# Performance work log

Measured on AMD Instinct MI355X. Metric: run time of the kernel, lower is better.

The kernel has to match this reference:

```python
import jax, jax.numpy as jnp
import numpy as np

B_, L_, H_ = 8, 512, 768
DIN, N, R, K = 1536, 64, 48, 4  # d_inner, d_state, dt_rank, d_conv


def setup_inputs() -> dict:
    key = jax.random.key(0)
    ks = jax.random.split(key, 16)
    rn = lambda i, shp, sc=0.02: jax.random.normal(ks[i], shp, dtype=jnp.float32) * sc
    inp = {
        "text": jax.random.normal(ks[0], (B_, L_, H_), dtype=jnp.float32),
        "audio": jax.random.normal(ks[1], (B_, L_, H_), dtype=jnp.float32),
        "video": jax.random.normal(ks[2], (B_, L_, H_), dtype=jnp.float32),
        "proj_w": rn(3, (3 * H_, H_)),
        "proj_b": jnp.zeros((H_,), jnp.float32),
        "proj_ln_g": jnp.ones((H_,), jnp.float32),
        "proj_ln_b": jnp.zeros((H_,), jnp.float32),
        "blk_ln_g": jnp.ones((H_,), jnp.float32),
        "blk_ln_b": jnp.zeros((H_,), jnp.float32),
        "in_proj_w": rn(4, (H_, 2 * DIN)),
        "conv_w": rn(5, (DIN, 1, K), 0.1),
        "conv_b": jnp.zeros((DIN,), jnp.float32),
        "x_proj_w": rn(6, (DIN, R + 2 * N)),
        "dt_proj_w": rn(7, (R, DIN), 0.1),
        "dt_proj_b": jnp.full((DIN,), -4.6, jnp.float32),  # softplus -> ~0.01 dt
        "A_log": jnp.log(jnp.tile(jnp.arange(1, N + 1, dtype=jnp.float32), (DIN, 1))),
        "D": jnp.ones((DIN,), jnp.float32),
        "out_proj_w": rn(8, (DIN, H_)),
    }
    return inp


def _ln(x, g, b, eps=1e-5):
    mu = x.mean(-1, keepdims=True)
    xc = x - mu
    v = (xc * xc).mean(-1, keepdims=True)
    return xc * jax.lax.rsqrt(v + eps) * g + b


def _mamba(h, in_proj_w, conv_w, conv_b, x_proj_w, dt_proj_w, dt_proj_b, A_log, D, out_proj_w):
    Bsz, L, _ = h.shape
    xz = h @ in_proj_w                       # [B,L,2*DIN]
    x, z = jnp.split(xz, 2, axis=-1)         # each [B,L,DIN]
    # causal depthwise conv1d over time
    xc = jax.lax.conv_general_dilated(
        x.transpose(0, 2, 1), conv_w, (1,), [(K - 1, 0)],
        dimension_numbers=("NCH", "OIH", "NCH"), feature_group_count=DIN)
    x = jax.nn.silu(xc + conv_b[None, :, None]).transpose(0, 2, 1)  # [B,L,DIN]
    dbl = x @ x_proj_w                       # [B,L,R+2N]
    dt, Bm, Cm = jnp.split(dbl, [R, R + N], axis=-1)
    delta = jax.nn.softplus(dt @ dt_proj_w + dt_proj_b)  # [B,L,DIN]
    A = -jnp.exp(A_log)                      # [DIN,N]

    def step(hcar, t):
        d_t, b_t, c_t, u_t = t               # [B,DIN],[B,N],[B,N],[B,DIN]
        hcar = jnp.exp(d_t[..., None] * A) * hcar + (d_t * u_t)[..., None] * b_t[:, None, :]
        y = jnp.einsum("bdn,bn->bd", hcar, c_t)
        return hcar, y

    xs = (delta.transpose(1, 0, 2), Bm.transpose(1, 0, 2), Cm.transpose(1, 0, 2), x.transpose(1, 0, 2))
    h0 = jnp.zeros((Bsz, DIN, N), x.dtype)
    _, ys = jax.lax.scan(step, h0, xs)       # ys: [L,B,DIN]
    y = ys.transpose(1, 0, 2) + x * D
    y = y * jax.nn.silu(z)
    return y @ out_proj_w                    # [B,L,H]


def reference(text, audio, video, proj_w, proj_b, proj_ln_g, proj_ln_b,
              blk_ln_g, blk_ln_b, in_proj_w, conv_w, conv_b, x_proj_w,
              dt_proj_w, dt_proj_b, A_log, D, out_proj_w):
    fused = jnp.concatenate([text, audio, video], axis=-1) @ proj_w + proj_b
    fused = _ln(fused, proj_ln_g, proj_ln_b)
    m = _mamba(_ln(fused, blk_ln_g, blk_ln_b), in_proj_w, conv_w, conv_b,
               x_proj_w, dt_proj_w, dt_proj_b, A_log, D, out_proj_w)
    fused = fused + m                         # residual (dropout = identity in eval)
    return fused.mean(axis=1)                 # [B,H]
```

## Files before the change

kernel.cpp:

```cpp
#include <hip/hip_runtime.h>
#include <hip/hip_bf16.h>
#include <cstddef>
#include <cstdint>

#define DIN 1536
#define LSEQ 512

typedef __hip_bfloat16 bf16;
typedef __attribute__((ext_vector_type(8))) short short8x;
typedef __attribute__((ext_vector_type(4))) float f32x4;
typedef const __attribute__((address_space(1))) unsigned int* gp1;
typedef __attribute__((address_space(3))) unsigned int* lp3;

__device__ inline float readlane_f(float v, int l) {
  return __uint_as_float(__builtin_amdgcn_readlane(__float_as_uint(v), l));
}
__device__ inline void gload_lds(const bf16* g, unsigned short* l) {
  __builtin_amdgcn_global_load_lds((gp1)g, (lp3)l, 16, 0, 0);
}
__device__ inline void bsplit(float v, bf16& h, bf16& l) {
  h = __float2bfloat16(v);
  l = __float2bfloat16(v - __bfloat162float(h));
}
__device__ inline float softplusf(float t) {
  return fmaxf(t, 0.f) + log1pf(__expf(-fabsf(t)));
}
template<int CTRL>
__device__ inline float dpp_add(float v) {
  int t = __builtin_amdgcn_update_dpp(0, __float_as_int(v), CTRL, 0xf, 0xf, true);
  return v + __int_as_float(t);
}
__device__ inline float dpp_wave_sum(float p) {
  p = dpp_add<0x111>(p);
  p = dpp_add<0x112>(p);
  p = dpp_add<0x114>(p);
  p = dpp_add<0x118>(p);
  p = dpp_add<0x142>(p);
  p = dpp_add<0x143>(p);
  return p;
}

template<int TBM, int TBN, int WR, int WC, int AMODE, int EPI>
__global__ __launch_bounds__(WR*WC*64) void mgemm(
    const bf16* __restrict__ Ah0, const bf16* __restrict__ Al0,
    const bf16* __restrict__ Ah1, const bf16* __restrict__ Al1,
    const bf16* __restrict__ Ah2, const bf16* __restrict__ Al2,
    const bf16* __restrict__ Bh, const bf16* __restrict__ Bl,
    const float* __restrict__ bias,
    float* __restrict__ C, float* __restrict__ C2,
    bf16* __restrict__ Oh, bf16* __restrict__ Ol,
    int K, int lda, int ldc)
{
  constexpr int NW = WR * WC;
  constexpr int SM = TBM / WR, SN = TBN / WC;
  constexpr int T_M = SM / 16, T_N = SN / 16;
  __shared__ unsigned short sAh[TBM * 32], sAl[TBM * 32];
  __shared__ unsigned short sBh[TBN * 32], sBl[TBN * 32];
  const int tid = threadIdx.x;
  const int lane = tid & 63, wid = tid >> 6;
  const int bm = blockIdx.x * TBM, bn = blockIdx.y * TBN;
  const int wr = wid / WC, wc = wid % WC;

  const int stg_m = lane >> 2;
  const int stg_k = ((lane & 3) ^ ((lane >> 3) & 3)) * 8;
  const int fo = (lane & 15) * 64 + ((((lane >> 4) ^ ((lane >> 1) & 3)) & 3) * 16);

  f32x4 acc[T_M][T_N];
  #pragma unroll
  for (int i = 0; i < T_M; ++i)
    #pragma unroll
    for (int j = 0; j < T_N; ++j) acc[i][j] = (f32x4){0.f, 0.f, 0.f, 0.f};

  for (int k0 = 0; k0 < K; k0 += 32) {
    __syncthreads();
    const bf16* pAh; const bf16* pAl; int ka;
    if (AMODE == 1) {
      int seg = k0 / 768;
      pAh = (seg == 0) ? Ah0 : (seg == 1) ? Ah1 : Ah2;
      pAl = (seg == 0) ? Al0 : (seg == 1) ? Al1 : Al2;
      ka = k0 - seg * 768;
    } else { pAh = Ah0; pAl = Al0; ka = k0; }
    #pragma unroll
    for (int q = wid; q < TBM / 16; q += NW) {
      size_t go = (size_t)(bm + q * 16 + stg_m) * lda + ka + stg_k;
      gload_lds(pAh + go, &sAh[q * 512]);
      gload_lds(pAl + go, &sAl[q * 512]);
    }
    #pragma unroll
    for (int q = wid; q < TBN / 16; q += NW) {
      size_t go = (size_t)(bn + q * 16 + stg_m) * K + k0 + stg_k;
      gload_lds(Bh + go, &sBh[q * 512]);
      gload_lds(Bl + go, &sBl[q * 512]);
    }
    __syncthreads();

    short8x ah[T_M], al[T_M], bh[T_N], bl[T_N];
    #pragma unroll
    for (int mi = 0; mi < T_M; ++mi) {
      int off = (wr * SM + mi * 16) * 64 + fo;
      ah[mi] = *(const short8x*)((const char*)sAh + off);
      al[mi] = *(const short8x*)((const char*)sAl + off);
    }
    #pragma unroll
    for (int nj = 0; nj < T_N; ++nj) {
      int off = (wc * SN + nj * 16) * 64 + fo;
      bh[nj] = *(const short8x*)((const char*)sBh + off);
      bl[nj] = *(const short8x*)((const char*)sBl + off);
    }
    #pragma unroll
    for (int mi = 0; mi < T_M; ++mi)
      #pragma unroll
      for (int nj = 0; nj < T_N; ++nj) {
        acc[mi][nj] = __builtin_amdgcn_mfma_f32_16x16x32_bf16(ah[mi], bh[nj], acc[mi][nj], 0, 0, 0);
        acc[mi][nj] = __builtin_amdgcn_mfma_f32_16x16x32_bf16(ah[mi], bl[nj], acc[mi][nj], 0, 0, 0);
        acc[mi][nj] = __builtin_amdgcn_mfma_f32_16x16x32_bf16(al[mi], bh[nj], acc[mi][nj], 0, 0, 0);
      }
  }

  const int cl = lane & 15, qd = lane >> 4;
  const int colbase = bn + wc * SN;
  const int rowbase = bm + wr * SM;
  if (EPI == 1) {
    #pragma unroll
    for (int mi = 0; mi < T_M; ++mi) {
      int r0 = rowbase + mi * 16 + qd * 4;
      #pragma unroll
      for (int nj = 0; nj < T_N; ++nj) {
        int col = colbase + nj * 16 + cl;
        float bv = bias[col];
        #pragma unroll
        for (int rg = 0; rg < 4; ++rg)
          C[(size_t)(r0 + rg) * ldc + col] = acc[mi][nj][rg] + bv;
      }
    }
  } else if (EPI == 4) {
    #pragma unroll
    for (int mi = 0; mi < T_M; ++mi) {
      int m = rowbase + mi * 16 + qd * 4;
      int b = m >> 9, l = m & 511;
      #pragma unroll
      for (int nj = 0; nj < T_N; ++nj) {
        int col = colbase + nj * 16 + cl;
        float bv = bias[col];
        float4 v;
        v.x = softplusf(acc[mi][nj][0] + bv);
        v.y = softplusf(acc[mi][nj][1] + bv);
        v.z = softplusf(acc[mi][nj][2] + bv);
        v.w = softplusf(acc[mi][nj][3] + bv);
        *reinterpret_cast<float4*>(&C[((size_t)b * DIN + col) * LSEQ + l]) = v;
      }
    }
  } else if (EPI == 5) {
    if (bn < 1536) {
      #pragma unroll
      for (int mi = 0; mi < T_M; ++mi) {
        int r0 = rowbase + mi * 16 + qd * 4;
        #pragma unroll
        for (int nj = 0; nj < T_N; ++nj) {
          int col = colbase + nj * 16 + cl;
          #pragma unroll
          for (int rg = 0; rg < 4; ++rg)
            C[(size_t)(r0 + rg) * ldc + col] = acc[mi][nj][rg];
        }
      }
    } else {
      #pragma unroll
      for (int mi = 0; mi < T_M; ++mi) {
        int m = rowbase + mi * 16 + qd * 4;
        int b = m >> 9, l = m & 511;
        #pragma unroll
        for (int nj = 0; nj < T_N; ++nj) {
          int colz = colbase - 1536 + nj * 16 + cl;
          float4 v;
          v.x = acc[mi][nj][0]; v.y = acc[mi][nj][1];
          v.z = acc[mi][nj][2]; v.w = acc[mi][nj][3];
          *reinterpret_cast<float4*>(&C2[((size_t)b * DIN + colz) * LSEQ + l]) = v;
        }
      }
    }
  } else if (EPI == 6) {
    #pragma unroll
    for (int mi = 0; mi < T_M; ++mi) {
      int r0 = rowbase + mi * 16 + qd * 4;
      #pragma unroll
      for (int nj = 0; nj < T_N; ++nj) {
        int col = colbase + nj * 16 + cl;
        #pragma unroll
        for (int rg = 0; rg < 4; ++rg) {
          float v = acc[mi][nj][rg];
          C[(size_t)(r0 + rg) * 192 + col] = v;
          if (col < 64) {
            bf16 h, l;
            if (col < 48) bsplit(v, h, l);
            else { h = __float2bfloat16(0.f); l = h; }
            Oh[(size_t)(r0 + rg) * 64 + col] = h;
            Ol[(size_t)(r0 + rg) * 64 + col] = l;
          }
        }
      }
    }
  }
}

__global__ __launch_bounds__(256) void split3_k(
    const float* __restrict__ s0, const float* __restrict__ s1,
    const float* __restrict__ s2, bf16* __restrict__ dst)
{
  const int per = 4096 * 768 / 256;
  int seg = blockIdx.x / per;
  int idx = (blockIdx.x - seg * per) * 256 + threadIdx.x;
  const float* src = (seg == 0) ? s0 : (seg == 1) ? s1 : s2;
  bf16* hi = dst + (size_t)seg * 2 * 4096 * 768;
  bf16* lo = hi + (size_t)4096 * 768;
  bf16 h, l; bsplit(src[idx], h, l);
  hi[idx] = h; lo[idx] = l;
}

__global__ __launch_bounds__(256) void wprep_k(
    const float* __restrict__ pw, const float* __restrict__ ipw,
    const float* __restrict__ xpw, const float* __restrict__ dtw,
    bf16* pwTh, bf16* pwTl, bf16* ipTh, bf16* ipTl,
    bf16* xpTh, bf16* xpTl, bf16* dtTh, bf16* dtTl)
{
  __shared__ float T[64][65];
  const int id = blockIdx.x, tid = threadIdx.x;
  const float* src; bf16 *hi, *lo; int P, Q, ld, Ppad, px, qx;
  if (id < 432)       { src = pw;  hi = pwTh; lo = pwTl; P = 2304; Q = 768;  ld = 768;  Ppad = 2304; px = id % 36;          qx = id / 36; }
  else if (id < 1008) { int i = id - 432;  src = ipw; hi = ipTh; lo = ipTl; P = 768;  Q = 3072; ld = 3072; Ppad = 768;  px = i % 12; qx = i / 12; }
  else if (id < 1080) { int i = id - 1008; src = xpw; hi = xpTh; lo = xpTl; P = 1536; Q = 176;  ld = 176;  Ppad = 1536; px = i % 24; qx = i / 24; }
  else                { int i = id - 1080; src = dtw; hi = dtTh; lo = dtTl; P = 48;   Q = 1536; ld = 1536; Ppad = 64;   px = 0;      qx = i; }
  const int p0 = px * 64, q0 = qx * 64;
  {
    int j = tid & 63, i0 = tid >> 6;
    for (int i = i0; i < 64; i += 4) {
      int p = p0 + i, q = q0 + j;
      T[i][j] = (p < P && q < Q) ? src[(size_t)p * ld + q] : 0.f;
    }
  }
  __syncthreads();
  {
    int ii = tid & 63, j0 = tid >> 6;
    for (int jj = j0; jj < 64; jj += 4) {
      bf16 h, l; bsplit(T[ii][jj], h, l);
      size_t o = (size_t)(q0 + jj) * Ppad + p0 + ii;
      hi[o] = h; lo[o] = l;
    }
  }
}

__device__ inline float block_sum256(float s, float* red) {
  #pragma unroll
  for (int o = 32; o > 0; o >>= 1) s += __shfl_xor(s, o, 64);
  int tid = threadIdx.x;
  __syncthreads();
  if ((tid & 63) == 0) red[tid >> 6] = s;
  __syncthreads();
  return red[0] + red[1] + red[2] + red[3];
}

__global__ __launch_bounds__(256) void ln2_k(
    const float* __restrict__ pre,
    const float* __restrict__ g1, const float* __restrict__ b1,
    const float* __restrict__ g2, const float* __restrict__ b2,
    float* __restrict__ fused, bf16* __restrict__ hAh, bf16* __restrict__ hAl)
{
  __shared__ float red[4];
  const int row = blockIdx.x;
  const int tid = threadIdx.x;
  const float* x = pre + (size_t)row * 768;
  float v0 = x[tid], v1 = x[tid + 256], v2 = x[tid + 512];

  float mu = block_sum256(v0 + v1 + v2, red) * (1.f / 768.f);
  float c0 = v0 - mu, c1 = v1 - mu, c2 = v2 - mu;
  float var = block_sum256(c0*c0 + c1*c1 + c2*c2, red) * (1.f / 768.f);
  float r = rsqrtf(var + 1e-5f);
  float f0 = c0 * r * g1[tid] + b1[tid];
  float f1 = c1 * r * g1[tid + 256] + b1[tid + 256];
  float f2 = c2 * r * g1[tid + 512] + b1[tid + 512];
  float* fo = fused + (size_t)row * 768;
  fo[tid] = f0; fo[tid + 256] = f1; fo[tid + 512] = f2;

  float mu2 = block_sum256(f0 + f1 + f2, red) * (1.f / 768.f);
  float d0 = f0 - mu2, d1 = f1 - mu2, d2 = f2 - mu2;
  float var2 = block_sum256(d0*d0 + d1*d1 + d2*d2, red) * (1.f / 768.f);
  float r2 = rsqrtf(var2 + 1e-5f);
  float h0 = d0 * r2 * g2[tid] + b2[tid];
  float h1 = d1 * r2 * g2[tid + 256] + b2[tid + 256];
  float h2 = d2 * r2 * g2[tid + 512] + b2[tid + 512];
  bf16 hh, hl;
  size_t o = (size_t)row * 768;
  bsplit(h0, hh, hl); hAh[o + tid] = hh; hAl[o + tid] = hl;
  bsplit(h1, hh, hl); hAh[o + tid + 256] = hh; hAl[o + tid + 256] = hl;
  bsplit(h2, hh, hl); hAh[o + tid + 512] = hh; hAl[o + tid + 512] = hl;
}

__global__ __launch_bounds__(256) void conv2x_k(
    const float* __restrict__ xbuf, const float* __restrict__ w,
    const float* __restrict__ cb, float* __restrict__ xct,
    bf16* __restrict__ xcAh, bf16* __restrict__ xcAl)
{
  __shared__ float Xs[67][65];
  __shared__ float Ys[64][65];
  const int tid = threadIdx.x;
  const int l0 = blockIdx.x * 64;
  const int d0 = blockIdx.y * 64;
  const int b  = blockIdx.z;
  for (int e = tid; e < 67 * 64; e += 256) {
    int r = e >> 6, dd = e & 63;
    int l = l0 - 3 + r;
    Xs[r][dd] = (l >= 0) ? xbuf[((size_t)b * 512 + l) * DIN + d0 + dd] : 0.f;
  }
  __syncthreads();
  {
    const int lane = tid & 63, grp = tid >> 6;
    #pragma unroll
    for (int i = 0; i < 16; ++i) {
      int dd = grp + i * 4;
      int d = d0 + dd;
      float acc = cb[d];
      #pragma unroll
      for (int k = 0; k < 4; ++k)
        acc = fmaf(Xs[lane + k][dd], w[d * 4 + k], acc);
      float v = acc / (1.f + __expf(-acc));
      xct[((size_t)b * DIN + d) * LSEQ + l0 + lane] = v;
      Ys[lane][dd] = v;
    }
  }
  __syncthreads();
  {
    const int dd = tid & 63, lg = tid >> 6;
    #pragma unroll
    for (int j = 0; j < 16; ++j) {
      int l = lg * 16 + j;
      bf16 h, lo; bsplit(Ys[l][dd], h, lo);
      size_t o = (size_t)(b * 512 + l0 + l) * DIN + d0 + dd;
      xcAh[o] = h; xcAl[o] = lo;
    }
  }
}

__global__ __launch_bounds__(256) void scan4_k(
    const float* __restrict__ delta_t, const float* __restrict__ xct,
    const float* __restrict__ dbl, const float* __restrict__ zt,
    const float* __restrict__ A_log, const float* __restrict__ Dv,
    float* __restrict__ ysbar)
{
  __shared__ float BC[64][128];
  const int tid = threadIdx.x;
  const int lane = tid & 63;
  const int wv = tid >> 6;
  const int bid = blockIdx.x;
  const int b = bid / 384;
  const int d = (bid - b * 384) * 4 + wv;
  const float Ad = -__expf(A_log[d * 64 + lane]);
  const float Dd = Dv[d];
  const size_t strm = ((size_t)b * DIN + d) * LSEQ;
  float h = 0.f;
  float ysum = 0.f;

  for (int l0 = 0; l0 < LSEQ; l0 += 64) {
    __syncthreads();
    #pragma unroll
    for (int i = 0; i < 16; ++i) {
      int t = wv * 16 + i;
      const float* src = dbl + (size_t)(b * LSEQ + l0 + t) * 192;
      float2 v; v.x = src[48 + lane]; v.y = src[112 + lane];
      *reinterpret_cast<float2*>(&BC[t][lane * 2]) = v;
    }
    float dt_v = delta_t[strm + l0 + lane];
    float u_v  = xct[strm + l0 + lane];
    float z_v  = zt[strm + l0 + lane];
    float du_v = dt_v * u_v;
    __syncthreads();

    float yk = 0.f;
    #pragma unroll
    for (int t2 = 0; t2 < 32; ++t2) {
      const int t0 = 2 * t2, t1 = t0 + 1;
      float dta = readlane_f(dt_v, t0), dua = readlane_f(du_v, t0);
      float dtb = readlane_f(dt_v, t1), dub = readlane_f(du_v, t1);
      float2 bca = *reinterpret_cast<const float2*>(&BC[t0][lane * 2]);
      float2 bcb = *reinterpret_cast<const float2*>(&BC[t1][lane * 2]);
      float ea = __expf(dta * Ad);
      float eb = __expf(dtb * Ad);
      h = fmaf(ea, h, dua * bca.x);
      float pa = h * bca.y;
      h = fmaf(eb, h, dub * bcb.x);
      float pb = h * bcb.y;
      pa = dpp_add<0x111>(pa); pb = dpp_add<0x111>(pb);
      pa = dpp_add<0x112>(pa); pb = dpp_add<0x112>(pb);
      pa = dpp_add<0x114>(pa); pb = dpp_add<0x114>(pb);
      pa = dpp_add<0x118>(pa); pb = dpp_add<0x118>(pb);
      pa = dpp_add<0x142>(pa); pb = dpp_add<0x142>(pb);
      pa = dpp_add<0x143>(pa); pb = dpp_add<0x143>(pb);
      float ta_ = readlane_f(pa, 63);
      float tb_ = readlane_f(pb, 63);
      yk = (lane == t0) ? ta_ : yk;
      yk = (lane == t1) ? tb_ : yk;
    }
    float yv = (yk + u_v * Dd) * (z_v / (1.f + __expf(-z_v)));
    ysum += yv;
  }
  float tot = readlane_f(dpp_wave_sum(ysum), 63);
  if (lane == 0) ysbar[b * 1536 + d] = tot;
}

__global__ __launch_bounds__(256) void final_k(
    const float* __restrict__ fused, const float* __restrict__ ysbar,
    const float* __restrict__ W, float* __restrict__ out)
{
  __shared__ float ys[1536];
  const int b = blockIdx.y;
  const int c = blockIdx.x * 256 + threadIdx.x;
  for (int i = threadIdx.x; i < 1536; i += 256) ys[i] = ysbar[b * 1536 + i];
  __syncthreads();
  float sf = 0.f;
  for (int l = 0; l < 512; ++l) sf += fused[(size_t)((b << 9) + l) * 768 + c];
  float dot = 0.f;
  for (int d = 0; d < 1536; ++d) dot = fmaf(ys[d], W[(size_t)d * 768 + c], dot);
  out[b * 768 + c] = (sf + dot) * (1.f / 512.f);
}

extern "C" void kernel_launch(void* const* d_in, const int* in_sizes, int n_in,
                              void* d_out, int out_size, void* d_ws, size_t ws_size,
                              hipStream_t stream)
{
  const float* text      = (const float*)d_in[0];
  const float* audio     = (const float*)d_in[1];
  const float* video     = (const float*)d_in[2];
  const float* proj_w    = (const float*)d_in[3];
  const float* proj_b    = (const float*)d_in[4];
  const float* proj_ln_g = (const float*)d_in[5];
  const float* proj_ln_b = (const float*)d_in[6];
  const float* blk_ln_g  = (const float*)d_in[7];
  const float* blk_ln_b  = (const float*)d_in[8];
  const float* in_proj_w = (const float*)d_in[9];
  const float* conv_w    = (const float*)d_in[10];
  const float* conv_b    = (const float*)d_in[11];
  const float* x_proj_w  = (const float*)d_in[12];
  const float* dt_proj_w = (const float*)d_in[13];
  const float* dt_proj_b = (const float*)d_in[14];
  const float* A_log     = (const float*)d_in[15];
  const float* Dv        = (const float*)d_in[16];
  const float* out_projw = (const float*)d_in[17];
  float* out = (float*)d_out;

  char* p = (char*)d_ws;
  const size_t P768 = (size_t)4096 * 768 * 2;
  char* S1 = p; p += 6 * P768;
  char* SW = p; p += 18087936;
  char* S3 = p; p += (size_t)4096 * 768 * 4;
  char* S4 = p; p += (size_t)4096 * 768 * 4;
  char* S6 = p; p += (size_t)4096 * 1536 * 4;
  char* S7 = p; p += (size_t)4096 * 1536 * 4;
  char* S8 = p; p += (size_t)4096 * 1536 * 4;
  char* SD = p; p += (size_t)4096 * 64 * 4;
  char* S9 = p; p += (size_t)4096 * 192 * 4;
  char* SY = p; p += 12288 * 4;

  bf16* modspl = (bf16*)S1;
  bf16 *tAh = (bf16*)S1,              *tAl = (bf16*)(S1 + P768);
  bf16 *aAh = (bf16*)(S1 + 2 * P768), *aAl = (bf16*)(S1 + 3 * P768);
  bf16 *vAh = (bf16*)(S1 + 4 * P768), *vAl = (bf16*)(S1 + 5 * P768);
  bf16 *hAh = (bf16*)S1,              *hAl = (bf16*)(S1 + P768);
  bf16 *xcAh = (bf16*)S1,             *xcAl = (bf16*)(S1 + (size_t)4096 * 1536 * 2);
  bf16 *pwTh = (bf16*)SW,                    *pwTl = pwTh + (size_t)768 * 2304;
  bf16 *ipTh = pwTl + (size_t)768 * 2304,    *ipTl = ipTh + (size_t)3072 * 768;
  bf16 *xpTh = ipTl + (size_t)3072 * 768,    *xpTl = xpTh + (size_t)192 * 1536;
  bf16 *dtTh = xpTl + (size_t)192 * 1536,    *dtTl = dtTh + (size_t)1536 * 64;
  float* pre     = (float*)S3;
  float* fused   = (float*)S4;
  float* xbuf    = (float*)S6;  float* delta_t = (float*)S6;
  float* zt      = (float*)S7;
  float* xct     = (float*)S8;
  bf16 *dtAh = (bf16*)SD, *dtAl = (bf16*)(SD + (size_t)4096 * 64 * 2);
  float* dbl     = (float*)S9;
  float* ysbar   = (float*)SY;

  split3_k<<<36864, 256, 0, stream>>>(text, audio, video, modspl);
  wprep_k<<<1104, 256, 0, stream>>>(proj_w, in_proj_w, x_proj_w, dt_proj_w,
                                    pwTh, pwTl, ipTh, ipTl, xpTh, xpTl, dtTh, dtTl);
  mgemm<128, 64, 4, 2, 1, 1><<<dim3(32, 12), 512, 0, stream>>>(
      tAh, tAl, aAh, aAl, vAh, vAl, pwTh, pwTl, proj_b,
      pre, nullptr, nullptr, nullptr, 2304, 768, 768);
  ln2_k<<<4096, 256, 0, stream>>>(pre, proj_ln_g, proj_ln_b, blk_ln_g, blk_ln_b, fused, hAh, hAl);
  mgemm<128, 128, 2, 2, 0, 5><<<dim3(32, 24), 256, 0, stream>>>(
      hAh, hAl, nullptr, nullptr, nullptr, nullptr, ipTh, ipTl, nullptr,
      xbuf, zt, nullptr, nullptr, 768, 768, 1536);
  conv2x_k<<<dim3(8, 24, 8), 256, 0, stream>>>(xbuf, conv_w, conv_b, xct, xcAh, xcAl);
  mgemm<64, 64, 4, 2, 0, 6><<<dim3(64, 3), 512, 0, stream>>>(
      xcAh, xcAl, nullptr, nullptr, nullptr, nullptr, xpTh, xpTl, nullptr,
      dbl, nullptr, dtAh, dtAl, 1536, 1536, 192);
  mgemm<128, 64, 4, 2, 0, 4><<<dim3(32, 24), 512, 0, stream>>>(
      dtAh, dtAl, nullptr, nullptr, nullptr, nullptr, dtTh, dtTl, dt_proj_b,
      delta_t, nullptr, nullptr, nullptr, 64, 64, 0);
  scan4_k<<<3072, 256, 0, stream>>>(delta_t, xct, dbl, zt, A_log, Dv, ysbar);
  final_k<<<dim3(3, 8), 256, 0, stream>>>(fused, ysbar, out_projw, out);
}
```

Measured before the change: 673.7 us.

## Restructure scan reduction via LDS partial sums and merge prep kernels

The scan kernel stops doing a full 64-lane DPP reduction plus readlane at every timestep. It now does a 2-step row reduction to groups of 4 lanes and writes the partials to shared memory, then each lane sums its own timestep's 16 partials after the chunk. Delta and delta*u are staged in LDS instead of being read with readlane, and exp is replaced by exp2 with a prescaled A. Separately, the split and weight-prep kernels are merged into one launch to save a launch. This trades a long serial DPP chain per step for extra LDS writes and reads.

```diff
diff --git a/kernel.cpp b/kernel.cpp
--- a/kernel.cpp
+++ b/kernel.cpp
@@ -202,28 +202,28 @@
   }
 }
 
-__global__ __launch_bounds__(256) void split3_k(
+__global__ __launch_bounds__(256) void prep_k(
     const float* __restrict__ s0, const float* __restrict__ s1,
-    const float* __restrict__ s2, bf16* __restrict__ dst)
-{
-  const int per = 4096 * 768 / 256;
-  int seg = blockIdx.x / per;
-  int idx = (blockIdx.x - seg * per) * 256 + threadIdx.x;
-  const float* src = (seg == 0) ? s0 : (seg == 1) ? s1 : s2;
-  bf16* hi = dst + (size_t)seg * 2 * 4096 * 768;
-  bf16* lo = hi + (size_t)4096 * 768;
-  bf16 h, l; bsplit(src[idx], h, l);
-  hi[idx] = h; lo[idx] = l;
-}
-
-__global__ __launch_bounds__(256) void wprep_k(
+    const float* __restrict__ s2, bf16* __restrict__ moddst,
     const float* __restrict__ pw, const float* __restrict__ ipw,
     const float* __restrict__ xpw, const float* __restrict__ dtw,
     bf16* pwTh, bf16* pwTl, bf16* ipTh, bf16* ipTl,
     bf16* xpTh, bf16* xpTl, bf16* dtTh, bf16* dtTl)
 {
   __shared__ float T[64][65];
-  const int id = blockIdx.x, tid = threadIdx.x;
+  const int tid = threadIdx.x;
+  if (blockIdx.x < 36864) {
+    const int per = 4096 * 768 / 256;
+    int seg = blockIdx.x / per;
+    int idx = (blockIdx.x - seg * per) * 256 + tid;
+    const float* src = (seg == 0) ? s0 : (seg == 1) ? s1 : s2;
+    bf16* hi = moddst + (size_t)seg * 2 * 4096 * 768;
+    bf16* lo = hi + (size_t)4096 * 768;
+    bf16 h, l; bsplit(src[idx], h, l);
+    hi[idx] = h; lo[idx] = l;
+    return;
+  }
+  const int id = blockIdx.x - 36864;
   const float* src; bf16 *hi, *lo; int P, Q, ld, Ppad, px, qx;
   if (id < 432)       { src = pw;  hi = pwTh; lo = pwTl; P = 2304; Q = 768;  ld = 768;  Ppad = 2304; px = id % 36;          qx = id / 36; }
   else if (id < 1008) { int i = id - 432;  src = ipw; hi = ipTh; lo = ipTl; P = 768;  Q = 3072; ld = 3072; Ppad = 768;  px = i % 12; qx = i / 12; }
@@ -339,24 +339,25 @@
   }
 }
 
-__global__ __launch_bounds__(256) void scan4_k(
+__global__ __launch_bounds__(256) void scan5_k(
     const float* __restrict__ delta_t, const float* __restrict__ xct,
     const float* __restrict__ dbl, const float* __restrict__ zt,
     const float* __restrict__ A_log, const float* __restrict__ Dv,
     float* __restrict__ ysbar)
 {
   __shared__ float BC[64][128];
+  __shared__ float DT[4][64][2];
+  __shared__ float Pq[4][64][17];
   const int tid = threadIdx.x;
   const int lane = tid & 63;
   const int wv = tid >> 6;
   const int bid = blockIdx.x;
   const int b = bid / 384;
   const int d = (bid - b * 384) * 4 + wv;
-  const float Ad = -__expf(A_log[d * 64 + lane]);
+  const float Ad2 = -__expf(A_log[d * 64 + lane]) * 1.442695041f;
   const float Dd = Dv[d];
   const size_t strm = ((size_t)b * DIN + d) * LSEQ;
-  float h = 0.f;
-  float ysum = 0.f;
+  float h = 0.f, ysum = 0.f;
 
   for (int l0 = 0; l0 < LSEQ; l0 += 64) {
     __syncthreads();
@@ -370,34 +371,24 @@
     float dt_v = delta_t[strm + l0 + lane];
     float u_v  = xct[strm + l0 + lane];
     float z_v  = zt[strm + l0 + lane];
-    float du_v = dt_v * u_v;
+    float2 dd; dd.x = dt_v; dd.y = dt_v * u_v;
+    *reinterpret_cast<float2*>(&DT[wv][lane][0]) = dd;
     __syncthreads();
 
+    #pragma unroll
+    for (int t = 0; t < 64; ++t) {
+      float2 sd = *reinterpret_cast<const float2*>(&DT[wv][t][0]);
+      float2 bc = *reinterpret_cast<const float2*>(&BC[t][lane * 2]);
+      float e = exp2f(sd.x * Ad2);
+      h = fmaf(e, h, sd.y * bc.x);
+      float p = h * bc.y;
+      p = dpp_add<0x111>(p);
+      p = dpp_add<0x112>(p);
+      if ((lane & 3) == 3) Pq[wv][t][lane >> 2] = p;
+    }
     float yk = 0.f;
     #pragma unroll
-    for (int t2 = 0; t2 < 32; ++t2) {
-      const int t0 = 2 * t2, t1 = t0 + 1;
-      float dta = readlane_f(dt_v, t0), dua = readlane_f(du_v, t0);
-      float dtb = readlane_f(dt_v, t1), dub = readlane_f(du_v, t1);
-      float2 bca = *reinterpret_cast<const float2*>(&BC[t0][lane * 2]);
-      float2 bcb = *reinterpret_cast<const float2*>(&BC[t1][lane * 2]);
-      float ea = __expf(dta * Ad);
-      float eb = __expf(dtb * Ad);
-      h = fmaf(ea, h, dua * bca.x);
-      float pa = h * bca.y;
-      h = fmaf(eb, h, dub * bcb.x);
-      float pb = h * bcb.y;
-      pa = dpp_add<0x111>(pa); pb = dpp_add<0x111>(pb);
-      pa = dpp_add<0x112>(pa); pb = dpp_add<0x112>(pb);
-      pa = dpp_add<0x114>(pa); pb = dpp_add<0x114>(pb);
-      pa = dpp_add<0x118>(pa); pb = dpp_add<0x118>(pb);
-      pa = dpp_add<0x142>(pa); pb = dpp_add<0x142>(pb);
-      pa = dpp_add<0x143>(pa); pb = dpp_add<0x143>(pb);
-      float ta_ = readlane_f(pa, 63);
-      float tb_ = readlane_f(pb, 63);
-      yk = (lane == t0) ? ta_ : yk;
-      yk = (lane == t1) ? tb_ : yk;
-    }
+    for (int j = 0; j < 16; ++j) yk += Pq[wv][lane][j];
     float yv = (yk + u_v * Dd) * (z_v / (1.f + __expf(-z_v)));
     ysum += yv;
   }
@@ -477,8 +468,8 @@
   float* dbl     = (float*)S9;
   float* ysbar   = (float*)SY;
 
-  split3_k<<<36864, 256, 0, stream>>>(text, audio, video, modspl);
-  wprep_k<<<1104, 256, 0, stream>>>(proj_w, in_proj_w, x_proj_w, dt_proj_w,
+  prep_k<<<37968, 256, 0, stream>>>(text, audio, video, modspl,
+                                    proj_w, in_proj_w, x_proj_w, dt_proj_w,
                                     pwTh, pwTl, ipTh, ipTl, xpTh, xpTl, dtTh, dtTl);
   mgemm<128, 64, 4, 2, 1, 1><<<dim3(32, 12), 512, 0, stream>>>(
       tAh, tAl, aAh, aAl, vAh, vAl, pwTh, pwTl, proj_b,
@@ -494,6 +485,6 @@
   mgemm<128, 64, 4, 2, 0, 4><<<dim3(32, 24), 512, 0, stream>>>(
       dtAh, dtAl, nullptr, nullptr, nullptr, nullptr, dtTh, dtTl, dt_proj_b,
       delta_t, nullptr, nullptr, nullptr, 64, 64, 0);
-  scan4_k<<<3072, 256, 0, stream>>>(delta_t, xct, dbl, zt, A_log, Dv, ysbar);
+  scan5_k<<<3072, 256, 0, stream>>>(delta_t, xct, dbl, zt, A_log, Dv, ysbar);
   final_k<<<dim3(3, 8), 256, 0, stream>>>(fused, ysbar, out_projw, out);
 }
```

Result: no change. 663.7 us (-1.5%).
